# Kernel optimization log

Hardware: AMD Instinct MI355X
Metric: run time of the kernel (lower is better)

The kernel has to match this reference:

```python
import jax, jax.numpy as jnp
import numpy as np
from jax import lax

N, E, DIN, D, L, H, T, NE = 20000, 240000, 768, 256, 3, 4, 9, 8  # nodes, edges, input_dim, gnn_dim, layers, heads, tags, n_etype
DH = D // H
BN_EPS = 1e-5

def _bn(x, g, b):
    # eval-mode BatchNorm1d with running stats (mean=0, var=1)
    return x * (g / np.sqrt(1.0 + BN_EPS)) + b

def _gelu(x):
    return jax.nn.gelu(x, approximate=False)

def setup_inputs():
    key = jax.random.key(0)
    ks = iter(jax.random.split(key, 48))
    nrm = lambda shape: jax.random.normal(next(ks), shape, jnp.float32) * 0.02
    return {
        "node_emb": jax.random.normal(next(ks), (N, DIN), jnp.float32),
        "edge_index": jax.random.randint(next(ks), (2, E), 0, N),
        "edge_type": jax.random.randint(next(ks), (E,), 0, NE),
        "tag_gt": jax.random.randint(next(ks), (N,), 0, T),
        "W_lm2gnn": nrm((DIN, D)), "b_lm2gnn": jnp.zeros((D,)),
        "We1": nrm((L, NE + 1, D)), "be1": jnp.zeros((L, D)),
        "g1": jnp.ones((L, D)), "bb1": jnp.zeros((L, D)),
        "We2": nrm((L, D, D)), "be2": jnp.zeros((L, D)),
        "Wq": nrm((L, D, D)), "bq": jnp.zeros((L, D)),
        "Wk": nrm((L, 2 * D, D)), "bk": jnp.zeros((L, D)),
        "Wm": nrm((L, 2 * D, D)), "bm": jnp.zeros((L, D)),
        "Wp1": nrm((L, D, D)), "bp1": jnp.zeros((L, D)),
        "g2": jnp.ones((L, D)), "bb2": jnp.zeros((L, D)),
        "Wp2": nrm((L, D, D)), "bp2": jnp.zeros((L, D)),
        "Wo": nrm((D, D)), "bo": jnp.zeros((D,)),
        "Wc": nrm((D, D)), "bc": jnp.zeros((D,)),
        "Wt": nrm((D, T)), "bt": jnp.zeros((T,)),
        "crf_start": nrm((T,)), "crf_end": nrm((T,)), "crf_trans": nrm((T, T)),
    }

def _emissions(node_emb, edge_index, edge_type, W_lm2gnn, b_lm2gnn, We1, be1, g1, bb1,
               We2, be2, Wq, bq, Wk, bk, Wm, bm, Wp1, bp1, g2, bb2, Wp2, bp2,
               Wo, bo, Wc, bc, Wt, bt):
    H0 = _gelu(node_emb @ W_lm2gnn + b_lm2gnn)
    loop = jnp.arange(N)
    src = jnp.concatenate([edge_index[0], loop])          # (Etot,)
    dst = jnp.concatenate([edge_index[1], loop])
    # one-hot edge types + self-loop type NE
    ev = jnp.concatenate([jax.nn.one_hot(edge_type, NE + 1, dtype=jnp.float32),
                          jnp.zeros((N, NE + 1), jnp.float32).at[:, NE].set(1.0)], axis=0)
    deg = jax.ops.segment_sum(jnp.ones_like(src, jnp.float32), src, N)[src]  # src out-degree per edge
    X = H0
    for l in range(L):
        e = _bn(ev @ We1[l] + be1[l], g1[l], bb1[l])
        e = jax.nn.relu(e) @ We2[l] + be2[l]              # edge embeddings (Etot, D)
        x_i, x_j = X[dst], X[src]                          # target, source gathers
        q = (x_j @ Wq[l] + bq[l]).reshape(-1, H, DH)
        k = (x_i @ Wk[l][:D] + e @ Wk[l][D:] + bk[l]).reshape(-1, H, DH)
        m = (x_j @ Wm[l][:D] + e @ Wm[l][D:] + bm[l]).reshape(-1, H, DH)
        s = (q * k).sum(-1) / np.sqrt(DH)                  # (Etot, H)
        smax = jax.ops.segment_max(s, src, N)[src]
        ex = jnp.exp(s - smax)
        den = jax.ops.segment_sum(ex, src, N)[src]
        alpha = ex / (den + 1e-16) * deg[:, None]          # segment softmax over src, degree-scaled
        out_e = (m * alpha[:, :, None]).reshape(-1, D)
        aggr = jax.ops.segment_sum(out_e, dst, N)          # scatter-add to targets
        Xl = _bn(aggr @ Wp1[l] + bp1[l], g2[l], bb2[l])
        X = _gelu(jax.nn.relu(Xl) @ Wp2[l] + bp2[l])       # mlp then activation (dropout = eval identity)
    hidden = _gelu((H0 @ Wo + bo) + (X @ Wc + bc))
    return hidden @ Wt + bt                                # (N, T)

def reference(node_emb, edge_index, edge_type, tag_gt, W_lm2gnn, b_lm2gnn, We1, be1, g1, bb1,
              We2, be2, Wq, bq, Wk, bk, Wm, bm, Wp1, bp1, g2, bb2, Wp2, bp2,
              Wo, bo, Wc, bc, Wt, bt, crf_start, crf_end, crf_trans):
    em = _emissions(node_emb, edge_index, edge_type, W_lm2gnn, b_lm2gnn, We1, be1, g1, bb1,
                    We2, be2, Wq, bq, Wk, bk, Wm, bm, Wp1, bp1, g2, bb2, Wp2, bp2,
                    Wo, bo, Wc, bc, Wt, bt)
    # CRF Viterbi decode (batch=1, full-length mask)
    def vstep(score, em_t):
        cand = score[:, None] + crf_trans                  # (T, T)
        return jnp.max(cand, axis=0) + em_t, jnp.argmax(cand, axis=0)
    last, bps = lax.scan(vstep, crf_start + em[0], em[1:])
    last_tag = jnp.argmax(last + crf_end)
    def back(t, bp_t):
        prev = bp_t[t]
        return prev, prev
    _, prevs = lax.scan(back, last_tag, bps, reverse=True)
    path = jnp.concatenate([prevs, last_tag[None]])
    return path[None, :]                                   # (1, N) best tag sequence
```

## Files before the change

### kernel.cpp

```cpp
#include <hip/hip_runtime.h>

#define NN 20000
#define EE 240000
#define ETOTAL 260000
#define DIN 768
#define DD 256
#define NT 9

typedef __attribute__((ext_vector_type(2))) float f32x2;

__device__ __forceinline__ float gelu_f(float x) {
  return 0.5f * x * (1.0f + erff(x * 0.70710678118654752440f));
}

#define VSTEP_CORE(EIN, SIN, SOUT)                                        \
  asm volatile(                                                           \
    "s_nop 2\n\t"                                                         \
    "v_readlane_b32 s84, %[sv], 0\n\t"                                    \
    "v_readlane_b32 s85, %[sv], 1\n\t"                                    \
    "v_readlane_b32 s86, %[sv], 2\n\t"                                    \
    "v_readlane_b32 s87, %[sv], 3\n\t"                                    \
    "v_readlane_b32 s88, %[sv], 4\n\t"                                    \
    "v_readlane_b32 s89, %[sv], 5\n\t"                                    \
    "v_readlane_b32 s90, %[sv], 6\n\t"                                    \
    "v_readlane_b32 s91, %[sv], 7\n\t"                                    \
    "v_readlane_b32 s92, %[sv], 8\n\t"                                    \
    "v_pk_add_f32 v[80:81], s[84:85], %[u01]\n\t"                         \
    "v_pk_add_f32 v[82:83], s[86:87], %[u23]\n\t"                         \
    "v_pk_add_f32 v[84:85], s[88:89], %[u45]\n\t"                         \
    "v_pk_add_f32 v[86:87], s[90:91], %[u67]\n\t"                         \
    "v_add_f32 v88, s92, %[u8]\n\t"                                       \
    "v_max3_f32 v80, v80, v81, v82\n\t"                                   \
    "v_max3_f32 v83, v83, v84, v85\n\t"                                   \
    "v_max3_f32 v86, v86, v87, v88\n\t"                                   \
    "v_max3_f32 v80, v80, v83, v86\n\t"                                   \
    "v_add_f32 %[out], v80, %[e]\n\t"                                     \
    : [out]"=v"(SOUT)                                                     \
    : [sv]"v"(SIN), [e]"v"(EIN),                                          \
      [u01]"v"(tc01), [u23]"v"(tc23), [u45]"v"(tc45), [u67]"v"(tc67),     \
      [u8]"v"(tcol8)                                                      \
    : "s84","s85","s86","s87","s88","s89","s90","s91","s92",              \
      "v80","v81","v82","v83","v84","v85","v86","v87","v88")

#define RUN8(E0, E1) do {                                                 \
  float s0, s1, s2, s3, s4, s5, s6, s7;                                   \
  VSTEP_CORE((E0).x, s, s0); VSTEP_CORE((E0).y, s0, s1);                  \
  VSTEP_CORE((E0).z, s1, s2); VSTEP_CORE((E0).w, s2, s3);                 \
  float4 stq0; stq0.x = s0; stq0.y = s1; stq0.z = s2; stq0.w = s3;        \
  *(float4*)svp = stq0;                                                   \
  VSTEP_CORE((E1).x, s3, s4); VSTEP_CORE((E1).y, s4, s5);                 \
  VSTEP_CORE((E1).z, s5, s6); VSTEP_CORE((E1).w, s6, s7);                 \
  float4 stq1; stq1.x = s4; stq1.y = s5; stq1.z = s6; stq1.w = s7;        \
  *(float4*)(svp + 256) = stq1;                                           \
  s = s7; svp += 512;                                                     \
} while (0)

__global__ __launch_bounds__(256) void gemm_k(
    const float* __restrict__ A, const float* __restrict__ B,
    const float* __restrict__ bias,
    const float* __restrict__ bng, const float* __restrict__ bnb,
    float* __restrict__ C, int M, int K, int N, int act)
{
  __shared__ float As[32][64];
  __shared__ float Bs[32][64];
  const int tid = threadIdx.x;
  const int tx = tid & 15, ty = tid >> 4;
  const int m0 = blockIdx.y * 64, n0 = blockIdx.x * 64;
  float acc[4][4];
#pragma unroll
  for (int i = 0; i < 4; ++i)
#pragma unroll
    for (int j = 0; j < 4; ++j) acc[i][j] = 0.f;

  for (int kk = 0; kk < K; kk += 32) {
#pragma unroll
    for (int L = tid; L < 512; L += 256) {
      int r = L >> 3, c4 = L & 7;
      int gm = m0 + r;
      float4 v = make_float4(0.f, 0.f, 0.f, 0.f);
      if (gm < M) v = *(const float4*)(A + (size_t)gm * K + kk + c4 * 4);
      As[c4 * 4 + 0][r] = v.x; As[c4 * 4 + 1][r] = v.y;
      As[c4 * 4 + 2][r] = v.z; As[c4 * 4 + 3][r] = v.w;
    }
#pragma unroll
    for (int L = tid; L < 512; L += 256) {
      int r = L >> 4, c4 = L & 15;
      *(float4*)&Bs[r][c4 * 4] = *(const float4*)(B + (size_t)(kk + r) * N + n0 + c4 * 4);
    }
    __syncthreads();
#pragma unroll
    for (int k = 0; k < 32; ++k) {
      float a[4], b[4];
      *(float4*)a = *(const float4*)&As[k][ty * 4];
      *(float4*)b = *(const float4*)&Bs[k][tx * 4];
#pragma unroll
      for (int i = 0; i < 4; ++i)
#pragma unroll
        for (int j = 0; j < 4; ++j) acc[i][j] += a[i] * b[j];
    }
    __syncthreads();
  }
  const float bnc = 0.99999500003749968752f;
#pragma unroll
  for (int i = 0; i < 4; ++i) {
    int gm = m0 + ty * 4 + i;
    if (gm >= M) continue;
    float o[4];
#pragma unroll
    for (int j = 0; j < 4; ++j) {
      int n = n0 + tx * 4 + j;
      float x = acc[i][j];
      if (bias) x += bias[n];
      if (act == 1) x = gelu_f(x);
      else if (act == 2) { x = x * (bng[n] * bnc) + bnb[n]; x = fmaxf(x, 0.f); }
      o[j] = x;
    }
    *(float4*)(C + (size_t)gm * N + n0 + tx * 4) = *(const float4*)o;
  }
}

__global__ __launch_bounds__(256) void gemm3_k(
    const float* __restrict__ A, const float* __restrict__ B0,
    const float* __restrict__ bias0, const float* __restrict__ B1,
    const float* __restrict__ B2, float* __restrict__ C0,
    float* __restrict__ C1, float* __restrict__ C2, int M)
{
  __shared__ float As[32][64];
  __shared__ float Bs[3][32][64];
  const int tid = threadIdx.x;
  const int tx = tid & 15, ty = tid >> 4;
  const int m0 = blockIdx.y * 64, n0 = blockIdx.x * 64;
  float acc0[4][4], acc1[4][4], acc2[4][4];
#pragma unroll
  for (int i = 0; i < 4; ++i)
#pragma unroll
    for (int j = 0; j < 4; ++j) { acc0[i][j] = 0.f; acc1[i][j] = 0.f; acc2[i][j] = 0.f; }

  for (int kk = 0; kk < DD; kk += 32) {
#pragma unroll
    for (int L = tid; L < 512; L += 256) {
      int r = L >> 3, c4 = L & 7;
      int gm = m0 + r;
      float4 v = make_float4(0.f, 0.f, 0.f, 0.f);
      if (gm < M) v = *(const float4*)(A + (size_t)gm * DD + kk + c4 * 4);
      As[c4 * 4 + 0][r] = v.x; As[c4 * 4 + 1][r] = v.y;
      As[c4 * 4 + 2][r] = v.z; As[c4 * 4 + 3][r] = v.w;
    }
#pragma unroll
    for (int L = tid; L < 1536; L += 256) {
      int which = L >> 9, r = (L >> 4) & 31, c4 = L & 15;
      const float* Bp = (which == 0) ? B0 : (which == 1) ? B1 : B2;
      *(float4*)&Bs[which][r][c4 * 4] =
          *(const float4*)(Bp + (size_t)(kk + r) * DD + n0 + c4 * 4);
    }
    __syncthreads();
#pragma unroll
    for (int k = 0; k < 32; ++k) {
      float a[4], b0[4], b1[4], b2[4];
      *(float4*)a = *(const float4*)&As[k][ty * 4];
      *(float4*)b0 = *(const float4*)&Bs[0][k][tx * 4];
      *(float4*)b1 = *(const float4*)&Bs[1][k][tx * 4];
      *(float4*)b2 = *(const float4*)&Bs[2][k][tx * 4];
#pragma unroll
      for (int i = 0; i < 4; ++i)
#pragma unroll
        for (int j = 0; j < 4; ++j) {
          acc0[i][j] += a[i] * b0[j];
          acc1[i][j] += a[i] * b1[j];
          acc2[i][j] += a[i] * b2[j];
        }
    }
    __syncthreads();
  }
#pragma unroll
  for (int i = 0; i < 4; ++i) {
    int gm = m0 + ty * 4 + i;
    if (gm >= M) continue;
    float o0[4], o1[4], o2[4];
#pragma unroll
    for (int j = 0; j < 4; ++j) {
      int n = n0 + tx * 4 + j;
      o0[j] = acc0[i][j] + bias0[n];
      o1[j] = acc1[i][j];
      o2[j] = acc2[i][j];
    }
    *(float4*)(C0 + (size_t)gm * DD + n0 + tx * 4) = *(const float4*)o0;
    *(float4*)(C1 + (size_t)gm * DD + n0 + tx * 4) = *(const float4*)o1;
    *(float4*)(C2 + (size_t)gm * DD + n0 + tx * 4) = *(const float4*)o2;
  }
}

__global__ __launch_bounds__(256) void gemm_cat_k(
    const float* __restrict__ A1, const float* __restrict__ B1,
    const float* __restrict__ bias1, const float* __restrict__ A2,
    const float* __restrict__ B2, const float* __restrict__ bias2,
    float* __restrict__ C, int M)
{
  __shared__ float As[32][64];
  __shared__ float Bs[32][64];
  const int tid = threadIdx.x;
  const int tx = tid & 15, ty = tid >> 4;
  const int m0 = blockIdx.y * 64, n0 = blockIdx.x * 64;
  float acc[4][4];
#pragma unroll
  for (int i = 0; i < 4; ++i)
#pragma unroll
    for (int j = 0; j < 4; ++j) acc[i][j] = 0.f;

  for (int kk = 0; kk < 2 * DD; kk += 32) {
    const float* Ap = (kk < DD) ? A1 : A2;
    const float* Bp = (kk < DD) ? B1 : B2;
    const int ko = kk & (DD - 1);
#pragma unroll
    for (int L = tid; L < 512; L += 256) {
      int r = L >> 3, c4 = L & 7;
      int gm = m0 + r;
      float4 v = make_float4(0.f, 0.f, 0.f, 0.f);
      if (gm < M) v = *(const float4*)(Ap + (size_t)gm * DD + ko + c4 * 4);
      As[c4 * 4 + 0][r] = v.x; As[c4 * 4 + 1][r] = v.y;
      As[c4 * 4 + 2][r] = v.z; As[c4 * 4 + 3][r] = v.w;
    }
#pragma unroll
    for (int L = tid; L < 512; L += 256) {
      int r = L >> 4, c4 = L & 15;
      *(float4*)&Bs[r][c4 * 4] = *(const float4*)(Bp + (size_t)(ko + r) * DD + n0 + c4 * 4);
    }
    __syncthreads();
#pragma unroll
    for (int k = 0; k < 32; ++k) {
      float a[4], b[4];
      *(float4*)a = *(const float4*)&As[k][ty * 4];
      *(float4*)b = *(const float4*)&Bs[k][tx * 4];
#pragma unroll
      for (int i = 0; i < 4; ++i)
#pragma unroll
        for (int j = 0; j < 4; ++j) acc[i][j] += a[i] * b[j];
    }
    __syncthreads();
  }
#pragma unroll
  for (int i = 0; i < 4; ++i) {
    int gm = m0 + ty * 4 + i;
    if (gm >= M) continue;
    float o[4];
#pragma unroll
    for (int j = 0; j < 4; ++j) {
      int n = n0 + tx * 4 + j;
      o[j] = gelu_f(acc[i][j] + bias1[n] + bias2[n]);
    }
    *(float4*)(C + (size_t)gm * DD + n0 + tx * 4) = *(const float4*)o;
  }
}

__global__ __launch_bounds__(256) void edge_tables_k(
    const float* __restrict__ We1l, const float* __restrict__ be1l,
    const float* __restrict__ g1l, const float* __restrict__ bb1l,
    const float* __restrict__ We2l, const float* __restrict__ be2l,
    const float* __restrict__ WkEl, const float* __restrict__ bkl,
    const float* __restrict__ WmEl, const float* __restrict__ bml,
    float* __restrict__ ketab, float* __restrict__ metab)
{
  __shared__ float r_s[DD];
  __shared__ float e_s[DD];
  const int t = blockIdx.x, d = threadIdx.x;
  const float bnc = 0.99999500003749968752f;
  float pre = We1l[t * DD + d] + be1l[d];
  float bnv = pre * (g1l[d] * bnc) + bb1l[d];
  r_s[d] = fmaxf(bnv, 0.f);
  __syncthreads();
  float acc = 0.f;
  for (int c = 0; c < DD; ++c) acc += r_s[c] * We2l[c * DD + d];
  e_s[d] = acc + be2l[d];
  __syncthreads();
  float ka = 0.f, ma = 0.f;
  for (int c = 0; c < DD; ++c) {
    float ec = e_s[c];
    ka += ec * WkEl[c * DD + d];
    ma += ec * WmEl[c * DD + d];
  }
  ketab[t * DD + d] = ka + bkl[d];
  metab[t * DD + d] = ma + bml[d];
}

__global__ void deg_k(const int* __restrict__ ei, int* __restrict__ cnt,
                      int* __restrict__ cnt_d)
{
  for (int e = blockIdx.x * blockDim.x + threadIdx.x; e < EE; e += gridDim.x * blockDim.x) {
    atomicAdd(&cnt[ei[e]], 1);
    atomicAdd(&cnt_d[ei[EE + e]], 1);
  }
}

__global__ __launch_bounds__(256) void scan_k(const int* __restrict__ c,
                                              int* __restrict__ offs)
{
  __shared__ int part[257];
  const int tid = threadIdx.x;
  const int CH = (NN + 255) / 256;
  int a = tid * CH, b = a + CH; if (b > NN) b = NN;
  int s = 0;
  for (int i = a; i < b; ++i) s += c[i];
  part[tid] = s;
  __syncthreads();
  if (tid == 0) {
    int r = 0;
    for (int i = 0; i < 256; ++i) { int v = part[i]; part[i] = r; r += v; }
    part[256] = r;
  }
  __syncthreads();
  int r = part[tid];
  for (int i = a; i < b; ++i) { offs[i] = r; r += c[i]; }
  if (tid == 255) offs[NN] = part[256];
}

__global__ void fill_k(const int* __restrict__ key, const int* __restrict__ offs,
                       int* __restrict__ fc, int* __restrict__ eix)
{
  for (int e = blockIdx.x * blockDim.x + threadIdx.x; e < EE; e += gridDim.x * blockDim.x) {
    int d = key[e];
    int p = offs[d] + atomicAdd(&fc[d], 1);
    eix[p] = e;
  }
}

__global__ void pack_k(const int* __restrict__ ei, const int* __restrict__ et,
                       const int* __restrict__ eix, const int* __restrict__ eix_s,
                       int2* __restrict__ srcte_d, int2* __restrict__ dstte_s)
{
  for (int o = blockIdx.x * blockDim.x + threadIdx.x; o < EE; o += gridDim.x * blockDim.x) {
    int e = eix[o];
    srcte_d[o] = make_int2(ei[e], (e << 4) | et[e]);
    int e2 = eix_s[o];
    dstte_s[o] = make_int2(ei[EE + e2], (e2 << 4) | et[e2]);
  }
}

__global__ __launch_bounds__(256) void score2_k(
    const float* __restrict__ Q, const float* __restrict__ Kn,
    const float* __restrict__ ketab, const int* __restrict__ offs_s,
    const int2* __restrict__ dstte_s, float* __restrict__ sbuf,
    float2* __restrict__ sd)
{
  __shared__ float ke_s[NT * DD];
  for (int i = threadIdx.x; i < NT * DD; i += 256) ke_s[i] = ketab[i];
  __syncthreads();
  const int lane = threadIdx.x & 63, wave = threadIdx.x >> 6;
  const int h = lane >> 4, sl = lane & 15;
  const float4* Q4 = (const float4*)Q;
  const float4* K4 = (const float4*)Kn;
  int src = blockIdx.x * 4 + wave;
  if (src >= NN) return;
  float4 q = Q4[src * 64 + lane];
  float mx, sum;
  {
    float4 k = K4[src * 64 + lane];
    float4 ke = *(const float4*)(ke_s + (NT - 1) * DD + lane * 4);
    float p = q.x * (k.x + ke.x) + q.y * (k.y + ke.y) +
              q.z * (k.z + ke.z) + q.w * (k.w + ke.w);
    p += __shfl_xor(p, 8); p += __shfl_xor(p, 4);
    p += __shfl_xor(p, 2); p += __shfl_xor(p, 1);
    float se = p * 0.125f;
    if (sl == 0) sbuf[(EE + src) * 4 + h] = se;
    mx = se; sum = 1.0f;
  }
  int o1 = offs_s[src + 1];
  for (int o = offs_s[src]; o < o1; ++o) {
    int2 dt = dstte_s[o];
    int dst = dt.x, e = dt.y >> 4, t = dt.y & 15;
    float4 k = K4[dst * 64 + lane];
    float4 ke = *(const float4*)(ke_s + t * DD + lane * 4);
    float p = q.x * (k.x + ke.x) + q.y * (k.y + ke.y) +
              q.z * (k.z + ke.z) + q.w * (k.w + ke.w);
    p += __shfl_xor(p, 8); p += __shfl_xor(p, 4);
    p += __shfl_xor(p, 2); p += __shfl_xor(p, 1);
    float se = p * 0.125f;
    if (sl == 0) sbuf[e * 4 + h] = se;
    float nm = fmaxf(mx, se);
    sum = sum * expf(mx - nm) + expf(se - nm);
    mx = nm;
  }
  if (sl == 0) sd[src * 4 + h] = make_float2(mx, sum);
}

__global__ __launch_bounds__(256) void aggr2_k(
    const float* __restrict__ Mn, const float* __restrict__ metab,
    const float* __restrict__ sbuf, const float2* __restrict__ sd,
    const int* __restrict__ cnt, const int* __restrict__ offs,
    const int2* __restrict__ srcte_d, float* __restrict__ aggr)
{
  __shared__ float me_s[NT * DD];
  for (int i = threadIdx.x; i < NT * DD; i += 256) me_s[i] = metab[i];
  __syncthreads();
  const int lane = threadIdx.x & 63, wave = threadIdx.x >> 6;
  const int h = lane >> 4;
  const float4* M4 = (const float4*)Mn;
  int dst = blockIdx.x * 4 + wave;
  if (dst >= NN) return;
  float4 acc;
  {
    float2 sdv = sd[dst * 4 + h];
    float ex = expf(sbuf[(EE + dst) * 4 + h] - sdv.x);
    float alpha = ex / (sdv.y + 1e-16f) * (float)(cnt[dst] + 1);
    float4 m = M4[dst * 64 + lane];
    float4 me = *(const float4*)(me_s + (NT - 1) * DD + lane * 4);
    acc.x = (m.x + me.x) * alpha; acc.y = (m.y + me.y) * alpha;
    acc.z = (m.z + me.z) * alpha; acc.w = (m.w + me.w) * alpha;
  }
  int o1 = offs[dst + 1];
  for (int o = offs[dst]; o < o1; ++o) {
    int2 st = srcte_d[o];
    int src = st.x, e = st.y >> 4, t = st.y & 15;
    float2 sdv = sd[src * 4 + h];
    float ex = expf(sbuf[e * 4 + h] - sdv.x);
    float alpha = ex / (sdv.y + 1e-16f) * (float)(cnt[src] + 1);
    float4 m = M4[src * 64 + lane];
    float4 me = *(const float4*)(me_s + t * DD + lane * 4);
    acc.x += (m.x + me.x) * alpha; acc.y += (m.y + me.y) * alpha;
    acc.z += (m.z + me.z) * alpha; acc.w += (m.w + me.w) * alpha;
  }
  ((float4*)aggr)[dst * 64 + lane] = acc;
}

__global__ __launch_bounds__(256) void emis_k(
    const float* __restrict__ hidden, const float* __restrict__ Wt,
    const float* __restrict__ bt, float* __restrict__ em)
{
  __shared__ float wt_s[DD * NT];
  for (int i = threadIdx.x; i < DD * NT; i += 256) wt_s[i] = Wt[i];
  __syncthreads();
  const int lane = threadIdx.x & 63, wave = threadIdx.x >> 6;
  const float4* H4 = (const float4*)hidden;
  for (int n = blockIdx.x * 4 + wave; n < NN; n += gridDim.x * 4) {
    float4 h = H4[n * 64 + lane];
    const float* w0 = wt_s + (lane * 4) * NT;
    float p[NT];
#pragma unroll
    for (int t = 0; t < NT; ++t)
      p[t] = h.x * w0[t] + h.y * w0[NT + t] + h.z * w0[2 * NT + t] + h.w * w0[3 * NT + t];
#pragma unroll
    for (int m = 32; m >= 1; m >>= 1)
#pragma unroll
      for (int t = 0; t < NT; ++t) p[t] += __shfl_xor(p[t], m);
    if (lane == 0) {
#pragma unroll
      for (int t = 0; t < NT; ++t) em[n * NT + t] = p[t] + bt[t];
    }
  }
}

__global__ __launch_bounds__(256) void viterbi_k(
    const float* __restrict__ em, const float* __restrict__ cstart,
    const float* __restrict__ cend, const float* __restrict__ ctrans,
    float* __restrict__ sv, int* __restrict__ outp)
{
  const int VCS = 512;
  const int ST = VCS + 12;
  const int NCH = (NN + VCS - 1) / VCS;
  __shared__ float embufT[2][NT][VCS + 12];
  __shared__ float trT[NT * 16];
  __shared__ float scf[NT];
  __shared__ unsigned char fmaps[256][NT];
  __shared__ unsigned char ends_s[256];
  __shared__ int last_s;
  const int tid = threadIdx.x, lane = tid & 63, wave = tid >> 6;
  const int jl = min(lane & 15, NT - 1);

  for (int i = tid; i < VCS * NT; i += 256) {
    int t = i / NT, j = i - t * NT;
    embufT[0][j][t] = em[i];
  }
  if (tid < NT * NT) trT[(tid % NT) * 16 + (tid / NT)] = ctrans[tid];
  __syncthreads();

  f32x2 tc01, tc23, tc45, tc67;
  float tcol8 = 0.f;
  float s = 0.f;
  if (wave == 0) {
    tc01[0] = ctrans[0 * NT + jl]; tc01[1] = ctrans[1 * NT + jl];
    tc23[0] = ctrans[2 * NT + jl]; tc23[1] = ctrans[3 * NT + jl];
    tc45[0] = ctrans[4 * NT + jl]; tc45[1] = ctrans[5 * NT + jl];
    tc67[0] = ctrans[6 * NT + jl]; tc67[1] = ctrans[7 * NT + jl];
    tcol8   = ctrans[8 * NT + jl];
    s = cstart[jl] + embufT[0][jl][0];
    sv[lane * 4] = s;
  }

  for (int c = 0; c < NCH; ++c) {
    if (wave > 0) {
      if (c + 1 < NCH) {
        int base = (c + 1) * VCS * NT;
        int n2 = VCS * NT;
        if (base + n2 > NN * NT) n2 = NN * NT - base;
        float* dstb = &embufT[(c + 1) & 1][0][0];
        for (int i = tid - 64; i < n2; i += 192) {
          int t = i / NT, j = i - t * NT;
          dstb[j * ST + t] = em[base + i];
        }
      }
    } else {
      const float* ebT = &embufT[c & 1][0][0] + (size_t)jl * ST;
      int tbeg = (c == 0) ? 1 : c * VCS;
      int tend = (c + 1) * VCS; if (tend > NN) tend = NN;
      int off = tbeg - c * VCS;
      int nsteps = tend - tbeg;
      int pre = (8 - (tbeg & 7)) & 7; if (pre > nsteps) pre = nsteps;
      for (int i = 0; i < pre; ++i) {
        int t = tbeg + i;
        float e0 = ebT[off + i];
        float so;
        VSTEP_CORE(e0, s, so);
        s = so;
        sv[((size_t)t >> 2) * 256 + lane * 4 + (t & 3)] = s;
      }
      int rem = nsteps - pre;
      int ngr = rem >> 3;
      int tof = off + pre;
      float* svp = sv + ((size_t)(tbeg + pre) >> 2) * 256 + lane * 4;
      if (ngr > 0) {
        float4 eA0 = *(const float4*)&ebT[tof];
        float4 eA1 = *(const float4*)&ebT[tof + 4];
        float4 eB0, eB1;
        int g = 0;
        while (g + 2 <= ngr) {
          eB0 = *(const float4*)&ebT[tof + (g + 1) * 8];
          eB1 = *(const float4*)&ebT[tof + (g + 1) * 8 + 4];
          RUN8(eA0, eA1);
          eA0 = *(const float4*)&ebT[tof + (g + 2) * 8];
          eA1 = *(const float4*)&ebT[tof + (g + 2) * 8 + 4];
          RUN8(eB0, eB1);
          g += 2;
        }
        if (g < ngr) RUN8(eA0, eA1);
      }
      for (int i = pre + (ngr << 3); i < nsteps; ++i) {
        int t = tbeg + i;
        float e0 = ebT[off + i];
        float so;
        VSTEP_CORE(e0, s, so);
        s = so;
        sv[((size_t)t >> 2) * 256 + lane * 4 + (t & 3)] = s;
      }
    }
    __syncthreads();
  }

  if (wave == 0 && lane < NT) scf[lane] = s + cend[lane];
  __syncthreads();
  if (tid == 0) {
    float bv = scf[0]; int bi = 0;
    for (int j = 1; j < NT; ++j) if (scf[j] > bv) { bv = scf[j]; bi = j; }
    last_s = bi;
  }
  __syncthreads();

  const int RL = 79;
  int a = 1 + tid * RL;
  int b = a + RL; if (b > NN) b = NN;
  bool active = (a < NN);
  if (active) {
    int x[NT];
#pragma unroll
    for (int j = 0; j < NT; ++j) x[j] = j;
    for (int t = b - 1; t >= a; --t) {
      const float* sp = sv + ((size_t)(t - 1) >> 2) * 256 + ((t - 1) & 3);
      float sr[NT];
#pragma unroll
      for (int i = 0; i < NT; ++i) sr[i] = sp[i * 4];
#pragma unroll
      for (int j = 0; j < NT; ++j) {
        const float* tcx = trT + x[j] * 16;
        float bv = sr[0] + tcx[0]; int bi = 0;
#pragma unroll
        for (int i = 1; i < NT; ++i) {
          float cv = sr[i] + tcx[i];
          if (cv > bv) { bv = cv; bi = i; }
        }
        x[j] = bi;
      }
    }
#pragma unroll
    for (int j = 0; j < NT; ++j) fmaps[tid][j] = (unsigned char)x[j];
  }
  __syncthreads();
  if (tid == 0) {
    int x = last_s;
    for (int k = 255; k >= 0; --k) {
      ends_s[k] = (unsigned char)x;
      int ak = 1 + k * RL;
      if (ak < NN) x = fmaps[k][x];
    }
  }
  __syncthreads();
  if (active) {
    int x = ends_s[tid];
    outp[b - 1] = x;
    for (int t = b - 1; t >= a; --t) {
      const float* sp = sv + ((size_t)(t - 1) >> 2) * 256 + ((t - 1) & 3);
      const float* tcx = trT + x * 16;
      float bv = sp[0] + tcx[0]; int bi = 0;
#pragma unroll
      for (int i = 1; i < NT; ++i) {
        float cv = sp[i * 4] + tcx[i];
        if (cv > bv) { bv = cv; bi = i; }
      }
      x = bi;
      outp[t - 1] = x;
    }
  }
}

extern "C" void kernel_launch(void* const* d_in, const int* in_sizes, int n_in,
                              void* d_out, int out_size, void* d_ws, size_t ws_size,
                              hipStream_t stream)
{
  const float* node_emb = (const float*)d_in[0];
  const int* edge_index = (const int*)d_in[1];
  const int* edge_type = (const int*)d_in[2];
  const float* W_lm2gnn = (const float*)d_in[4];
  const float* b_lm2gnn = (const float*)d_in[5];
  const float* We1 = (const float*)d_in[6];
  const float* be1 = (const float*)d_in[7];
  const float* g1 = (const float*)d_in[8];
  const float* bb1 = (const float*)d_in[9];
  const float* We2 = (const float*)d_in[10];
  const float* be2 = (const float*)d_in[11];
  const float* Wq = (const float*)d_in[12];
  const float* bq = (const float*)d_in[13];
  const float* Wk = (const float*)d_in[14];
  const float* bk = (const float*)d_in[15];
  const float* Wm = (const float*)d_in[16];
  const float* bm = (const float*)d_in[17];
  const float* Wp1 = (const float*)d_in[18];
  const float* bp1 = (const float*)d_in[19];
  const float* g2 = (const float*)d_in[20];
  const float* bb2 = (const float*)d_in[21];
  const float* Wp2 = (const float*)d_in[22];
  const float* bp2 = (const float*)d_in[23];
  const float* Wo = (const float*)d_in[24];
  const float* bo = (const float*)d_in[25];
  const float* Wc = (const float*)d_in[26];
  const float* bc = (const float*)d_in[27];
  const float* Wt = (const float*)d_in[28];
  const float* bt = (const float*)d_in[29];
  const float* cstart = (const float*)d_in[30];
  const float* cend = (const float*)d_in[31];
  const float* ctrans = (const float*)d_in[32];

  const size_t NB = (size_t)NN * DD * sizeof(float);
  char* w = (char*)d_ws;
  float* H0 = (float*)(w + 0 * NB);
  float* Xb = (float*)(w + 1 * NB);
  float* Qb = (float*)(w + 2 * NB);
  float* Kb = (float*)(w + 3 * NB);
  float* Mb = (float*)(w + 4 * NB);
  char* sm = w + 5 * NB;
  size_t smo = 0;
  auto alloc = [&](size_t bytes) { char* p = sm + smo; smo += (bytes + 255) & ~255ull; return p; };
  float* sbuf = (float*)alloc((size_t)ETOTAL * 4 * 4);
  int* cnt = (int*)alloc((size_t)NN * 4);
  int* cnt_d = (int*)alloc((size_t)NN * 4);
  int* offs = (int*)alloc((size_t)(NN + 1) * 4);
  int* fc = (int*)alloc((size_t)NN * 4);
  int* offs_s = (int*)alloc((size_t)(NN + 1) * 4);
  int* fc_s = (int*)alloc((size_t)NN * 4);
  int* eix = (int*)alloc((size_t)EE * 4);
  int* eix_s = (int*)alloc((size_t)EE * 4);
  int2* srcte_d = (int2*)alloc((size_t)EE * 8);
  int2* dstte_s = (int2*)alloc((size_t)EE * 8);
  float2* sd = (float2*)alloc((size_t)NN * 4 * 8);
  float* ketab = (float*)alloc((size_t)NT * DD * 4);
  float* metab = (float*)alloc((size_t)NT * DD * 4);
  float* em = (float*)alloc((size_t)NN * NT * 4);
  float* sv = (float*)alloc(((size_t)NN * 64 + 256) * 4);
  const size_t needed = 5 * NB + smo;
  if (ws_size < needed) return;

  dim3 gg(DD / 64, (NN + 63) / 64);

  hipMemsetAsync(cnt, 0, (size_t)((char*)eix - (char*)cnt), stream);
  deg_k<<<1024, 256, 0, stream>>>(edge_index, cnt, cnt_d);
  scan_k<<<1, 256, 0, stream>>>(cnt_d, offs);
  scan_k<<<1, 256, 0, stream>>>(cnt, offs_s);
  fill_k<<<1024, 256, 0, stream>>>(edge_index + EE, offs, fc, eix);
  fill_k<<<1024, 256, 0, stream>>>(edge_index, offs_s, fc_s, eix_s);
  pack_k<<<1024, 256, 0, stream>>>(edge_index, edge_type, eix, eix_s,
                                   srcte_d, dstte_s);

  gemm_k<<<gg, 256, 0, stream>>>(node_emb, W_lm2gnn, b_lm2gnn, nullptr,
                                 nullptr, H0, NN, DIN, DD, 1);

  const float* Xcur = H0;
  for (int l = 0; l < 3; ++l) {
    edge_tables_k<<<NT, 256, 0, stream>>>(
        We1 + (size_t)l * NT * DD, be1 + l * DD, g1 + l * DD, bb1 + l * DD,
        We2 + (size_t)l * DD * DD, be2 + l * DD,
        Wk + (size_t)l * 2 * DD * DD + DD * DD, bk + l * DD,
        Wm + (size_t)l * 2 * DD * DD + DD * DD, bm + l * DD, ketab, metab);

    gemm3_k<<<gg, 256, 0, stream>>>(Xcur, Wq + (size_t)l * DD * DD, bq + l * DD,
                                    Wk + (size_t)l * 2 * DD * DD,
                                    Wm + (size_t)l * 2 * DD * DD,
                                    Qb, Kb, Mb, NN);

    score2_k<<<(NN + 3) / 4, 256, 0, stream>>>(Qb, Kb, ketab, offs_s,
                                               dstte_s, sbuf, sd);

    aggr2_k<<<(NN + 3) / 4, 256, 0, stream>>>(Mb, metab, sbuf, sd, cnt,
                                              offs, srcte_d, Kb);

    gemm_k<<<gg, 256, 0, stream>>>(Kb, Wp1 + (size_t)l * DD * DD, bp1 + l * DD,
                                   g2 + l * DD, bb2 + l * DD, Qb, NN, DD, DD, 2);
    gemm_k<<<gg, 256, 0, stream>>>(Qb, Wp2 + (size_t)l * DD * DD, bp2 + l * DD,
                                   nullptr, nullptr, Xb, NN, DD, DD, 1);
    Xcur = Xb;
  }

  gemm_cat_k<<<gg, 256, 0, stream>>>(H0, Wo, bo, Xb, Wc, bc, Qb, NN);

  emis_k<<<1250, 256, 0, stream>>>(Qb, Wt, bt, em);
  viterbi_k<<<1, 256, 0, stream>>>(em, cstart, cend, ctrans, sv, (int*)d_out);
}
```

Baseline: 2.647 ms.

## Double-buffer LDS tiles in GEMM kernels and batch edge-table precompute across layers

The gemm_k and gemm_cat_k kernels now use two LDS buffers and prefetch the next K-tile into registers while computing on the current one. This needs only one barrier per iteration and lets global loads overlap the FMA loop. Separately, the three per-layer edge_tables_k launches are merged into one 27-block launch before the layer loop, which writes per-layer tables and removes two small serial launches. The cost is double the LDS per block and extra registers for the prefetched tiles, which may lower occupancy.

```diff
diff --git a/kernel.cpp b/kernel.cpp
--- a/kernel.cpp
+++ b/kernel.cpp
@@ -61,45 +61,63 @@
     const float* __restrict__ bng, const float* __restrict__ bnb,
     float* __restrict__ C, int M, int K, int N, int act)
 {
-  __shared__ float As[32][64];
-  __shared__ float Bs[32][64];
+  __shared__ float As[2][32][64];
+  __shared__ float Bs[2][32][64];
   const int tid = threadIdx.x;
   const int tx = tid & 15, ty = tid >> 4;
   const int m0 = blockIdx.y * 64, n0 = blockIdx.x * 64;
+  const int rA0 = tid >> 3, cA0 = tid & 7;
+  const int rB0 = tid >> 4, cB0 = tid & 15;
+  const int gmA0 = m0 + rA0, gmA1 = m0 + rA0 + 32;
+  float4 a0, a1, b0, b1;
   float acc[4][4];
 #pragma unroll
   for (int i = 0; i < 4; ++i)
 #pragma unroll
     for (int j = 0; j < 4; ++j) acc[i][j] = 0.f;
 
-  for (int kk = 0; kk < K; kk += 32) {
-#pragma unroll
-    for (int L = tid; L < 512; L += 256) {
-      int r = L >> 3, c4 = L & 7;
-      int gm = m0 + r;
-      float4 v = make_float4(0.f, 0.f, 0.f, 0.f);
-      if (gm < M) v = *(const float4*)(A + (size_t)gm * K + kk + c4 * 4);
-      As[c4 * 4 + 0][r] = v.x; As[c4 * 4 + 1][r] = v.y;
-      As[c4 * 4 + 2][r] = v.z; As[c4 * 4 + 3][r] = v.w;
-    }
-#pragma unroll
-    for (int L = tid; L < 512; L += 256) {
-      int r = L >> 4, c4 = L & 15;
-      *(float4*)&Bs[r][c4 * 4] = *(const float4*)(B + (size_t)(kk + r) * N + n0 + c4 * 4);
-    }
+#define G_LOAD(kk) do {                                                     \
+    a0 = make_float4(0.f, 0.f, 0.f, 0.f); a1 = a0;                          \
+    if (gmA0 < M) a0 = *(const float4*)(A + (size_t)gmA0 * K + (kk) + cA0 * 4); \
+    if (gmA1 < M) a1 = *(const float4*)(A + (size_t)gmA1 * K + (kk) + cA0 * 4); \
+    b0 = *(const float4*)(B + (size_t)((kk) + rB0) * N + n0 + cB0 * 4);     \
+    b1 = *(const float4*)(B + (size_t)((kk) + rB0 + 16) * N + n0 + cB0 * 4);\
+  } while (0)
+#define L_WRITE(bf) do {                                                    \
+    As[bf][cA0 * 4 + 0][rA0] = a0.x; As[bf][cA0 * 4 + 1][rA0] = a0.y;       \
+    As[bf][cA0 * 4 + 2][rA0] = a0.z; As[bf][cA0 * 4 + 3][rA0] = a0.w;       \
+    As[bf][cA0 * 4 + 0][rA0 + 32] = a1.x; As[bf][cA0 * 4 + 1][rA0 + 32] = a1.y; \
+    As[bf][cA0 * 4 + 2][rA0 + 32] = a1.z; As[bf][cA0 * 4 + 3][rA0 + 32] = a1.w; \
+    *(float4*)&Bs[bf][rB0][cB0 * 4] = b0;                                   \
+    *(float4*)&Bs[bf][rB0 + 16][cB0 * 4] = b1;                              \
+  } while (0)
+#define COMPUTE(bf) do {                                                    \
+    _Pragma("unroll")                                                       \
+    for (int k = 0; k < 32; ++k) {                                          \
+      float a[4], b[4];                                                     \
+      *(float4*)a = *(const float4*)&As[bf][k][ty * 4];                     \
+      *(float4*)b = *(const float4*)&Bs[bf][k][tx * 4];                     \
+      _Pragma("unroll")                                                     \
+      for (int i = 0; i < 4; ++i)                                           \
+        _Pragma("unroll")                                                   \
+        for (int j = 0; j < 4; ++j) acc[i][j] += a[i] * b[j];               \
+    }                                                                       \
+  } while (0)
+
+  G_LOAD(0); L_WRITE(0); __syncthreads();
+  int buf = 0;
+  for (int kk = 32; kk < K; kk += 32) {
+    G_LOAD(kk);
+    COMPUTE(buf);
+    L_WRITE(buf ^ 1);
     __syncthreads();
-#pragma unroll
-    for (int k = 0; k < 32; ++k) {
-      float a[4], b[4];
-      *(float4*)a = *(const float4*)&As[k][ty * 4];
-      *(float4*)b = *(const float4*)&Bs[k][tx * 4];
-#pragma unroll
-      for (int i = 0; i < 4; ++i)
-#pragma unroll
-        for (int j = 0; j < 4; ++j) acc[i][j] += a[i] * b[j];
-    }
-    __syncthreads();
-  }
+    buf ^= 1;
+  }
+  COMPUTE(buf);
+#undef G_LOAD
+#undef L_WRITE
+#undef COMPUTE
+
   const float bnc = 0.99999500003749968752f;
 #pragma unroll
   for (int i = 0; i < 4; ++i) {
@@ -196,48 +214,66 @@
     const float* __restrict__ B2, const float* __restrict__ bias2,
     float* __restrict__ C, int M)
 {
-  __shared__ float As[32][64];
-  __shared__ float Bs[32][64];
+  __shared__ float As[2][32][64];
+  __shared__ float Bs[2][32][64];
   const int tid = threadIdx.x;
   const int tx = tid & 15, ty = tid >> 4;
   const int m0 = blockIdx.y * 64, n0 = blockIdx.x * 64;
+  const int rA0 = tid >> 3, cA0 = tid & 7;
+  const int rB0 = tid >> 4, cB0 = tid & 15;
+  const int gmA0 = m0 + rA0, gmA1 = m0 + rA0 + 32;
+  float4 a0, a1, b0, b1;
   float acc[4][4];
 #pragma unroll
   for (int i = 0; i < 4; ++i)
 #pragma unroll
     for (int j = 0; j < 4; ++j) acc[i][j] = 0.f;
 
-  for (int kk = 0; kk < 2 * DD; kk += 32) {
-    const float* Ap = (kk < DD) ? A1 : A2;
-    const float* Bp = (kk < DD) ? B1 : B2;
-    const int ko = kk & (DD - 1);
-#pragma unroll
-    for (int L = tid; L < 512; L += 256) {
-      int r = L >> 3, c4 = L & 7;
-      int gm = m0 + r;
-      float4 v = make_float4(0.f, 0.f, 0.f, 0.f);
-      if (gm < M) v = *(const float4*)(Ap + (size_t)gm * DD + ko + c4 * 4);
-      As[c4 * 4 + 0][r] = v.x; As[c4 * 4 + 1][r] = v.y;
-      As[c4 * 4 + 2][r] = v.z; As[c4 * 4 + 3][r] = v.w;
-    }
-#pragma unroll
-    for (int L = tid; L < 512; L += 256) {
-      int r = L >> 4, c4 = L & 15;
-      *(float4*)&Bs[r][c4 * 4] = *(const float4*)(Bp + (size_t)(ko + r) * DD + n0 + c4 * 4);
-    }
+#define G_LOAD(kk) do {                                                     \
+    const float* Ap = ((kk) < DD) ? A1 : A2;                                \
+    const float* Bp = ((kk) < DD) ? B1 : B2;                                \
+    const int ko = (kk) & (DD - 1);                                         \
+    a0 = make_float4(0.f, 0.f, 0.f, 0.f); a1 = a0;                          \
+    if (gmA0 < M) a0 = *(const float4*)(Ap + (size_t)gmA0 * DD + ko + cA0 * 4); \
+    if (gmA1 < M) a1 = *(const float4*)(Ap + (size_t)gmA1 * DD + ko + cA0 * 4); \
+    b0 = *(const float4*)(Bp + (size_t)(ko + rB0) * DD + n0 + cB0 * 4);     \
+    b1 = *(const float4*)(Bp + (size_t)(ko + rB0 + 16) * DD + n0 + cB0 * 4);\
+  } while (0)
+#define L_WRITE(bf) do {                                                    \
+    As[bf][cA0 * 4 + 0][rA0] = a0.x; As[bf][cA0 * 4 + 1][rA0] = a0.y;       \
+    As[bf][cA0 * 4 + 2][rA0] = a0.z; As[bf][cA0 * 4 + 3][rA0] = a0.w;       \
+    As[bf][cA0 * 4 + 0][rA0 + 32] = a1.x; As[bf][cA0 * 4 + 1][rA0 + 32] = a1.y; \
+    As[bf][cA0 * 4 + 2][rA0 + 32] = a1.z; As[bf][cA0 * 4 + 3][rA0 + 32] = a1.w; \
+    *(float4*)&Bs[bf][rB0][cB0 * 4] = b0;                                   \
+    *(float4*)&Bs[bf][rB0 + 16][cB0 * 4] = b1;                              \
+  } while (0)
+#define COMPUTE(bf) do {                                                    \
+    _Pragma("unroll")                                                       \
+    for (int k = 0; k < 32; ++k) {                                          \
+      float a[4], b[4];                                                     \
+      *(float4*)a = *(const float4*)&As[bf][k][ty * 4];                     \
+      *(float4*)b = *(const float4*)&Bs[bf][k][tx * 4];                     \
+      _Pragma("unroll")                                                     \
+      for (int i = 0; i < 4; ++i)                                           \
+        _Pragma("unroll")                                                   \
+        for (int j = 0; j < 4; ++j) acc[i][j] += a[i] * b[j];               \
+    }                                                                       \
+  } while (0)
+
+  G_LOAD(0); L_WRITE(0); __syncthreads();
+  int buf = 0;
+  for (int kk = 32; kk < 2 * DD; kk += 32) {
+    G_LOAD(kk);
+    COMPUTE(buf);
+    L_WRITE(buf ^ 1);
     __syncthreads();
-#pragma unroll
-    for (int k = 0; k < 32; ++k) {
-      float a[4], b[4];
-      *(float4*)a = *(const float4*)&As[k][ty * 4];
-      *(float4*)b = *(const float4*)&Bs[k][tx * 4];
-#pragma unroll
-      for (int i = 0; i < 4; ++i)
-#pragma unroll
-        for (int j = 0; j < 4; ++j) acc[i][j] += a[i] * b[j];
-    }
-    __syncthreads();
-  }
+    buf ^= 1;
+  }
+  COMPUTE(buf);
+#undef G_LOAD
+#undef L_WRITE
+#undef COMPUTE
+
 #pragma unroll
   for (int i = 0; i < 4; ++i) {
     int gm = m0 + ty * 4 + i;
@@ -252,25 +288,29 @@
   }
 }
 
-__global__ __launch_bounds__(256) void edge_tables_k(
-    const float* __restrict__ We1l, const float* __restrict__ be1l,
-    const float* __restrict__ g1l, const float* __restrict__ bb1l,
-    const float* __restrict__ We2l, const float* __restrict__ be2l,
-    const float* __restrict__ WkEl, const float* __restrict__ bkl,
-    const float* __restrict__ WmEl, const float* __restrict__ bml,
-    float* __restrict__ ketab, float* __restrict__ metab)
+__global__ __launch_bounds__(256) void edge_tables3_k(
+    const float* __restrict__ We1, const float* __restrict__ be1,
+    const float* __restrict__ g1, const float* __restrict__ bb1,
+    const float* __restrict__ We2, const float* __restrict__ be2,
+    const float* __restrict__ Wk, const float* __restrict__ bk,
+    const float* __restrict__ Wm, const float* __restrict__ bm,
+    float* __restrict__ ketab3, float* __restrict__ metab3)
 {
   __shared__ float r_s[DD];
   __shared__ float e_s[DD];
-  const int t = blockIdx.x, d = threadIdx.x;
+  const int l = blockIdx.x / NT, t = blockIdx.x - l * NT, d = threadIdx.x;
+  const float* We1l = We1 + (size_t)l * NT * DD;
+  const float* We2l = We2 + (size_t)l * DD * DD;
+  const float* WkEl = Wk + (size_t)l * 2 * DD * DD + DD * DD;
+  const float* WmEl = Wm + (size_t)l * 2 * DD * DD + DD * DD;
   const float bnc = 0.99999500003749968752f;
-  float pre = We1l[t * DD + d] + be1l[d];
-  float bnv = pre * (g1l[d] * bnc) + bb1l[d];
+  float pre = We1l[t * DD + d] + be1[l * DD + d];
+  float bnv = pre * (g1[l * DD + d] * bnc) + bb1[l * DD + d];
   r_s[d] = fmaxf(bnv, 0.f);
   __syncthreads();
   float acc = 0.f;
   for (int c = 0; c < DD; ++c) acc += r_s[c] * We2l[c * DD + d];
-  e_s[d] = acc + be2l[d];
+  e_s[d] = acc + be2[l * DD + d];
   __syncthreads();
   float ka = 0.f, ma = 0.f;
   for (int c = 0; c < DD; ++c) {
@@ -278,8 +318,8 @@
     ka += ec * WkEl[c * DD + d];
     ma += ec * WmEl[c * DD + d];
   }
-  ketab[t * DD + d] = ka + bkl[d];
-  metab[t * DD + d] = ma + bml[d];
+  ketab3[(size_t)l * NT * DD + t * DD + d] = ka + bk[l * DD + d];
+  metab3[(size_t)l * NT * DD + t * DD + d] = ma + bm[l * DD + d];
 }
 
 __global__ void deg_k(const int* __restrict__ ei, int* __restrict__ cnt,
@@ -668,8 +708,8 @@
   int2* srcte_d = (int2*)alloc((size_t)EE * 8);
   int2* dstte_s = (int2*)alloc((size_t)EE * 8);
   float2* sd = (float2*)alloc((size_t)NN * 4 * 8);
-  float* ketab = (float*)alloc((size_t)NT * DD * 4);
-  float* metab = (float*)alloc((size_t)NT * DD * 4);
+  float* ketab3 = (float*)alloc((size_t)3 * NT * DD * 4);
+  float* metab3 = (float*)alloc((size_t)3 * NT * DD * 4);
   float* em = (float*)alloc((size_t)NN * NT * 4);
   float* sv = (float*)alloc(((size_t)NN * 64 + 256) * 4);
   const size_t needed = 5 * NB + smo;
@@ -686,27 +726,24 @@
   pack_k<<<1024, 256, 0, stream>>>(edge_index, edge_type, eix, eix_s,
                                    srcte_d, dstte_s);
 
+  edge_tables3_k<<<3 * NT, 256, 0, stream>>>(We1, be1, g1, bb1, We2, be2,
+                                             Wk, bk, Wm, bm, ketab3, metab3);
+
   gemm_k<<<gg, 256, 0, stream>>>(node_emb, W_lm2gnn, b_lm2gnn, nullptr,
                                  nullptr, H0, NN, DIN, DD, 1);
 
   const float* Xcur = H0;
   for (int l = 0; l < 3; ++l) {
-    edge_tables_k<<<NT, 256, 0, stream>>>(
-        We1 + (size_t)l * NT * DD, be1 + l * DD, g1 + l * DD, bb1 + l * DD,
-        We2 + (size_t)l * DD * DD, be2 + l * DD,
-        Wk + (size_t)l * 2 * DD * DD + DD * DD, bk + l * DD,
-        Wm + (size_t)l * 2 * DD * DD + DD * DD, bm + l * DD, ketab, metab);
-
     gemm3_k<<<gg, 256, 0, stream>>>(Xcur, Wq + (size_t)l * DD * DD, bq + l * DD,
                                     Wk + (size_t)l * 2 * DD * DD,
                                     Wm + (size_t)l * 2 * DD * DD,
                                     Qb, Kb, Mb, NN);
 
-    score2_k<<<(NN + 3) / 4, 256, 0, stream>>>(Qb, Kb, ketab, offs_s,
-                                               dstte_s, sbuf, sd);
-
-    aggr2_k<<<(NN + 3) / 4, 256, 0, stream>>>(Mb, metab, sbuf, sd, cnt,
-                                              offs, srcte_d, Kb);
+    score2_k<<<(NN + 3) / 4, 256, 0, stream>>>(Qb, Kb, ketab3 + (size_t)l * NT * DD,
+                                               offs_s, dstte_s, sbuf, sd);
+
+    aggr2_k<<<(NN + 3) / 4, 256, 0, stream>>>(Mb, metab3 + (size_t)l * NT * DD,
+                                              sbuf, sd, cnt, offs, srcte_d, Kb);
 
     gemm_k<<<gg, 256, 0, stream>>>(Kb, Wp1 + (size_t)l * DD * DD, bp1 + l * DD,
                                    g2 + l * DD, bb2 + l * DD, Qb, NN, DD, DD, 2);
```

After: 2.908 ms. 9.9% more time.
